# Kernel optimization log

Hardware: AMD Instinct MI355X
Metric: run time of the kernel (lower is better)

The kernel has to match this reference:

```python
import jax, jax.numpy as jnp
import numpy as np

D = 512
H = 8
HD = D // H
EPS = 1e-8


def setup_inputs() -> dict:
    key = jax.random.key(0)
    ks = jax.random.split(key, 16)
    B, S = 4, 2048
    s = lambda n: 1.0 / np.sqrt(n)
    inp = {
        "gene_emb": jax.random.normal(ks[0], (B, S, D), jnp.float32),
        "expr_emb": jax.random.normal(ks[1], (B, S, D), jnp.float32),
        "M": jax.random.uniform(ks[2], (B, S, S), jnp.float32),
        # weights stored (in, out) so y = x @ W + b
        "W_fused": jax.random.normal(ks[3], (2 * D, D), jnp.float32) * s(2 * D),
        "b_fused": jnp.zeros((D,), jnp.float32),
        "W_Q": jax.random.normal(ks[4], (D, D), jnp.float32) * s(D),
        "b_Q": jnp.zeros((D,), jnp.float32),
        "W_K": jax.random.normal(ks[5], (D, D), jnp.float32) * s(D),
        "b_K": jnp.zeros((D,), jnp.float32),
        "W_V": jax.random.normal(ks[6], (D, D), jnp.float32) * s(D),
        "b_V": jnp.zeros((D,), jnp.float32),
        "W_O": jax.random.normal(ks[7], (D, D), jnp.float32) * s(D),
        "b_O": jnp.zeros((D,), jnp.float32),
    }
    return inp


def reference(gene_emb, expr_emb, M, W_fused, b_fused, W_Q, b_Q, W_K, b_K, W_V, b_V, W_O, b_O):
    B, S, _ = gene_emb.shape
    scale = HD ** (-0.5)
    fused = jnp.concatenate([gene_emb, expr_emb], axis=-1) @ W_fused + b_fused
    # (B,S,D) -> (B,H,S,HD)
    split = lambda x: x.reshape(B, S, H, HD).transpose(0, 2, 1, 3)
    Q = split(fused @ W_Q + b_Q)
    K = split(fused @ W_K + b_K)
    V = split(expr_emb @ W_V + b_V)
    scores = jnp.einsum("bhqd,bhkd->bhqk", Q, K) * scale
    Mg = M[:, None, :, :]  # broadcast over heads
    scores = scores * Mg
    attn = jax.nn.softmax(scores, axis=-1)
    A_sparse = attn * Mg
    norm = jnp.sum(jnp.abs(A_sparse), axis=-1, keepdims=True) + EPS
    A_bar = A_sparse / norm
    out = jnp.einsum("bhqk,bhkd->bhqd", A_bar, V)
    out = out.transpose(0, 2, 1, 3).reshape(B, S, D)
    return out @ W_O + b_O
```

## Files before the change

kernel.cpp:

```cpp
#include <hip/hip_runtime.h>

typedef unsigned short u16;
typedef __attribute__((ext_vector_type(8))) short bf16x8_t;
typedef __attribute__((ext_vector_type(4))) float f32x4_t;

__device__ __forceinline__ u16 f2bf(float x){
  union { float f; unsigned u; } v; v.f = x;
  unsigned r = v.u + 0x7FFFu + ((v.u >> 16) & 1u);
  return (u16)(r >> 16);
}
__device__ __forceinline__ float bf2f(u16 h){
  union { unsigned u; float f; } v; v.u = ((unsigned)h) << 16;
  return v.f;
}
__device__ __forceinline__ unsigned pack_hi16(float a, float b){
  union { float f; unsigned u; } x, y; x.f = a; y.f = b;
  return (x.u >> 16) | (y.u & 0xFFFF0000u);
}

__device__ __forceinline__ void gl2lds16(const u16* g, u16* l){
  __builtin_amdgcn_global_load_lds((const __attribute__((address_space(1))) void*)g,
                                   (__attribute__((address_space(3))) void*)l, 16, 0, 0);
}

__global__ __launch_bounds__(256) void split_concat_kernel(
    const float* __restrict__ gene, const float* __restrict__ expr,
    u16* __restrict__ Xh, u16* __restrict__ Xl)
{
  size_t e = ((size_t)blockIdx.x * 256 + threadIdx.x) * 4;
  int row = (int)(e >> 10);
  int col = (int)(e & 1023);
  const float* src = (col < 512) ? (gene + (size_t)row * 512 + col)
                                 : (expr + (size_t)row * 512 + (col - 512));
  float4 v = *(const float4*)src;
  float a[4] = {v.x, v.y, v.z, v.w};
  u16 hs[4], ls[4];
#pragma unroll
  for (int i = 0; i < 4; i++){
    hs[i] = f2bf(a[i]);
    ls[i] = f2bf(a[i] - bf2f(hs[i]));
  }
  *(uint2*)(Xh + e) = make_uint2(hs[0] | ((unsigned)hs[1] << 16), hs[2] | ((unsigned)hs[3] << 16));
  *(uint2*)(Xl + e) = make_uint2(ls[0] | ((unsigned)ls[1] << 16), ls[2] | ((unsigned)ls[3] << 16));
}

__global__ __launch_bounds__(256) void transpose_all_kernel(
    const float* __restrict__ Wf, const float* __restrict__ Wq,
    const float* __restrict__ Wk, const float* __restrict__ Wv,
    const float* __restrict__ Wo,
    u16* __restrict__ Wfth, u16* __restrict__ Wftl,
    u16* __restrict__ Wqth, u16* __restrict__ Wkth,
    u16* __restrict__ Wvth, u16* __restrict__ Woth)
{
  __shared__ float t[64][65];
  int id = blockIdx.x;
  const float* W; u16* Th; u16* Tl; int K, kx, ny;
  if (id < 128){ W = Wf; Th = Wfth; Tl = Wftl; K = 1024; kx = id >> 3; ny = id & 7; }
  else {
    int tt = id - 128; int wi = tt >> 6; tt &= 63; kx = tt >> 3; ny = tt & 7; K = 512;
    W  = (wi == 0) ? Wq  : (wi == 1) ? Wk  : (wi == 2) ? Wv  : Wo;
    Th = (wi == 0) ? Wqth: (wi == 1) ? Wkth: (wi == 2) ? Wvth: Woth;
    Tl = nullptr;
  }
  int k0 = kx * 64, n0 = ny * 64;
  int tid = threadIdx.x;
  int r = tid >> 4;
  int c4 = (tid & 15) * 4;
#pragma unroll
  for (int p = 0; p < 4; p++){
    int k = p * 16 + r;
    float4 v = *(const float4*)(W + (size_t)(k0 + k) * 512 + n0 + c4);
    t[c4 + 0][k] = v.x; t[c4 + 1][k] = v.y; t[c4 + 2][k] = v.z; t[c4 + 3][k] = v.w;
  }
  __syncthreads();
#pragma unroll
  for (int p = 0; p < 4; p++){
    int n = p * 16 + r;
    u16 hs[4], ls[4];
#pragma unroll
    for (int i = 0; i < 4; i++){
      float x = t[n][c4 + i];
      hs[i] = f2bf(x);
      ls[i] = f2bf(x - bf2f(hs[i]));
    }
    size_t o = (size_t)(n0 + n) * K + k0 + c4;
    *(uint2*)(Th + o) = make_uint2(hs[0] | ((unsigned)hs[1] << 16), hs[2] | ((unsigned)hs[3] << 16));
    if (Tl)
      *(uint2*)(Tl + o) = make_uint2(ls[0] | ((unsigned)ls[1] << 16), ls[2] | ((unsigned)ls[3] << 16));
  }
}

template<int SPLITS, int MODE, int DUAL>
__global__ __launch_bounds__(256, 2) void gemm_kernel(
    const u16* __restrict__ Ah, const u16* __restrict__ Al, int lda,
    const u16* __restrict__ Bh0, const u16* __restrict__ Bl0,
    const u16* __restrict__ Bh1, int K,
    const float* __restrict__ bias0, const float* __restrict__ bias1,
    void* __restrict__ out0, void* __restrict__ out1, void* __restrict__ outsec,
    float sc0, float sc1)
{
  __shared__ __align__(16) u16 sAh[128 * 32];
  __shared__ __align__(16) u16 sAl[SPLITS >= 2 ? 128 * 32 : 8];
  __shared__ __align__(16) u16 sBh[64 * 32];
  __shared__ __align__(16) u16 sBl[SPLITS == 3 ? 64 * 32 : 8];
  int tid = threadIdx.x;
  int lane = tid & 63, w = tid >> 6, quad = lane >> 4, l15 = lane & 15;
  int wm = w & 1, wn = w >> 1;
  int m0 = blockIdx.x * 128;
  int side = DUAL ? (int)(blockIdx.y >> 3) : 0;
  int n0 = (DUAL ? (int)(blockIdx.y & 7) : (int)blockIdx.y) * 64;
  const u16* Bh = (DUAL && side) ? Bh1 : Bh0;
  const float* bias = (DUAL && side) ? bias1 : bias0;
  void* o0 = (DUAL && side) ? outsec : out0;
  float sc = (DUAL && side) ? sc1 : sc0;

  f32x4_t acc[4][2];
#pragma unroll
  for (int i = 0; i < 4; i++)
#pragma unroll
    for (int j = 0; j < 2; j++)
#pragma unroll
      for (int r = 0; r < 4; r++) acc[i][j][r] = 0.f;

  int lrow = lane >> 2;
  int swzS = ((lane >> 2) & 3) ^ ((lane >> 4) & 3);
  int gkq  = ((lane & 3) ^ swzS) * 8;
  const u16* pAh0 = Ah + (size_t)(m0 + w * 32 + lrow) * lda + gkq;
  const u16* pAh1 = Ah + (size_t)(m0 + w * 32 + 16 + lrow) * lda + gkq;
  const u16* pAl0 = (SPLITS >= 2) ? Al + (size_t)(m0 + w * 32 + lrow) * lda + gkq : nullptr;
  const u16* pAl1 = (SPLITS >= 2) ? Al + (size_t)(m0 + w * 32 + 16 + lrow) * lda + gkq : nullptr;
  const u16* pBh0 = Bh + (size_t)(n0 + w * 16 + lrow) * K + gkq;
  const u16* pBl0 = (SPLITS == 3) ? Bl0 + (size_t)(n0 + w * 16 + lrow) * K + gkq : nullptr;
  u16* dAh = sAh + w * 1024;
  u16* dAl = sAl + w * 1024;
  u16* dBh = sBh + w * 512;
  u16* dBl = sBl + w * 512;

  int pq = (quad ^ ((l15 & 3) ^ ((l15 >> 2) & 3))) * 8;

  for (int k0 = 0; k0 < K; k0 += 32){
    __syncthreads();
    gl2lds16(pAh0 + k0, dAh);
    gl2lds16(pAh1 + k0, dAh + 512);
    if constexpr (SPLITS >= 2){
      gl2lds16(pAl0 + k0, dAl);
      gl2lds16(pAl1 + k0, dAl + 512);
    }
    gl2lds16(pBh0 + k0, dBh);
    if constexpr (SPLITS == 3)
      gl2lds16(pBl0 + k0, dBl);
    __syncthreads();

    bf16x8_t aH[4], aL[4], bH[2], bL[2];
#pragma unroll
    for (int mi = 0; mi < 4; mi++){
      int ad = (wm * 64 + mi * 16 + l15) * 32 + pq;
      aH[mi] = *(const bf16x8_t*)&sAh[ad];
      if constexpr (SPLITS >= 2) aL[mi] = *(const bf16x8_t*)&sAl[ad];
    }
#pragma unroll
    for (int ni = 0; ni < 2; ni++){
      int bd = (wn * 32 + ni * 16 + l15) * 32 + pq;
      bH[ni] = *(const bf16x8_t*)&sBh[bd];
      if constexpr (SPLITS == 3) bL[ni] = *(const bf16x8_t*)&sBl[bd];
    }
#pragma unroll
    for (int mi = 0; mi < 4; mi++)
#pragma unroll
      for (int ni = 0; ni < 2; ni++){
        acc[mi][ni] = __builtin_amdgcn_mfma_f32_16x16x32_bf16(aH[mi], bH[ni], acc[mi][ni], 0, 0, 0);
        if constexpr (SPLITS == 3)
          acc[mi][ni] = __builtin_amdgcn_mfma_f32_16x16x32_bf16(aH[mi], bL[ni], acc[mi][ni], 0, 0, 0);
        if constexpr (SPLITS >= 2)
          acc[mi][ni] = __builtin_amdgcn_mfma_f32_16x16x32_bf16(aL[mi], bH[ni], acc[mi][ni], 0, 0, 0);
      }
  }

#pragma unroll
  for (int mi = 0; mi < 4; mi++)
#pragma unroll
    for (int ni = 0; ni < 2; ni++){
      int gn = n0 + wn * 32 + ni * 16 + l15;
      float bs = bias[gn];
      int gm0 = m0 + wm * 64 + mi * 16 + quad * 4;
#pragma unroll
      for (int r = 0; r < 4; r++){
        float v = acc[mi][ni][r] + bs;
        int gm = gm0 + r;
        if constexpr (MODE == 0){
          u16 hb = f2bf(v);
          ((u16*)o0)[(size_t)gm * 512 + gn] = hb;
          ((u16*)out1)[(size_t)gm * 512 + gn] = f2bf(v - bf2f(hb));
        } else if constexpr (MODE == 1){
          ((u16*)o0)[(size_t)gm * 512 + gn] = f2bf(v * sc);
        } else if constexpr (MODE == 2){
          int bb = gm >> 11, s = gm & 2047;
          int hh = gn >> 6, d = gn & 63;
          ((u16*)o0)[((size_t)((bb * 8 + hh) * 64 + d) << 11) + s] = f2bf(v);
        } else {
          ((float*)o0)[(size_t)gm * 512 + gn] = v;
        }
      }
    }
}

__global__ __launch_bounds__(256, 3) void flash_kernel(
    const u16* __restrict__ Qh, const u16* __restrict__ Kh,
    const u16* __restrict__ Vt, const float* __restrict__ Mm,
    u16* __restrict__ Oh)
{
  __shared__ __align__(16) u16 sKh[64 * 64], sVt[64 * 64];
  int tid = threadIdx.x, lane = tid & 63, w = tid >> 6, quad = lane >> 4, l15 = lane & 15;
  int bh = blockIdx.y, b = bh >> 3, h = bh & 7;
  int q0 = blockIdx.x * 64;
  int q = q0 + w * 16 + l15;

  const u16* qp = Qh + ((size_t)(b * 2048 + q)) * 512 + h * 64 + quad * 8;
  bf16x8_t qH[2];
  qH[0] = *(const bf16x8_t*)qp;
  qH[1] = *(const bf16x8_t*)(qp + 32);

  int srow = lane >> 3;
  int gc = ((lane & 7) ^ (srow & 7)) * 8;
  const u16* gKh0 = Kh + ((size_t)(b * 2048 + w * 16 + srow)) * 512 + h * 64 + gc;
  const u16* gVt0 = Vt + ((size_t)(bh * 64 + w * 16 + srow)) * 2048 + gc;
  u16* dKh = sKh + w * 1024;
  u16* dVt = sVt + w * 1024;

  const float* mp = Mm + (size_t)b * (2048 * 2048) + (size_t)q * 2048 + quad * 8;

  float lp = 0.f;
  f32x4_t Oacc[4];
#pragma unroll
  for (int dn = 0; dn < 4; dn++)
#pragma unroll
    for (int r = 0; r < 4; r++) Oacc[dn][r] = 0.f;

  float Mc[2][8];
#pragma unroll
  for (int pt = 0; pt < 2; pt++){
    *(f32x4_t*)&Mc[pt][0] = *(const f32x4_t*)(mp + pt * 32);
    *(f32x4_t*)&Mc[pt][4] = *(const f32x4_t*)(mp + pt * 32 + 4);
  }

  int khi = l15 >> 2;
  int klo2 = (l15 & 3) * 2;
  int vlo = l15 & 7;
  int vhi = l15 >> 3;

  for (int k0 = 0; k0 < 2048; k0 += 64){
    __syncthreads();
    gl2lds16(gKh0 + (size_t)k0 * 512,       dKh);
    gl2lds16(gKh0 + (size_t)(k0 + 8) * 512, dKh + 512);
    gl2lds16(gVt0 + k0,                     dVt);
    gl2lds16(gVt0 + 8 * 2048 + k0,          dVt + 512);
    __syncthreads();

    float Mn[2][8];
    bool hasNext = (k0 + 64) < 2048;
    if (hasNext){
#pragma unroll
      for (int pt = 0; pt < 2; pt++){
        *(f32x4_t*)&Mn[pt][0] = *(const f32x4_t*)(mp + (k0 + 64) + pt * 32);
        *(f32x4_t*)&Mn[pt][4] = *(const f32x4_t*)(mp + (k0 + 64) + pt * 32 + 4);
      }
    }

    f32x4_t S[2][2];
#pragma unroll
    for (int pt = 0; pt < 2; pt++)
#pragma unroll
      for (int t = 0; t < 2; t++){
        int sr = klo2 + t;
        int base = (pt * 4 + khi) * 512 + sr * 64;
        f32x4_t s;
#pragma unroll
        for (int r = 0; r < 4; r++) s[r] = 0.f;
#pragma unroll
        for (int ds = 0; ds < 2; ds++){
          bf16x8_t kf = *(const bf16x8_t*)&sKh[base + (((ds * 4 + quad) ^ sr)) * 8];
          s = __builtin_amdgcn_mfma_f32_16x16x32_bf16(kf, qH[ds], s, 0, 0, 0);
        }
        S[pt][t] = s;
      }

#pragma unroll
    for (int pt = 0; pt < 2; pt++){
      float p[2][4];
#pragma unroll
      for (int t = 0; t < 2; t++)
#pragma unroll
        for (int r = 0; r < 4; r++){
          float m = Mc[pt][2 * r + t];
          float v = m * __builtin_amdgcn_exp2f(S[pt][t][r] * m);
          lp += v;
          p[t][r] = v;
        }
      union { unsigned u[4]; bf16x8_t v8; } pb;
#pragma unroll
      for (int r = 0; r < 4; r++)
        pb.u[r] = pack_hi16(p[0][r], p[1][r]);
#pragma unroll
      for (int dn = 0; dn < 4; dn++){
        bf16x8_t vf = *(const bf16x8_t*)&sVt[(dn * 2 + vhi) * 512 + vlo * 64 + (((pt * 4 + quad) ^ vlo)) * 8];
        Oacc[dn] = __builtin_amdgcn_mfma_f32_16x16x32_bf16(vf, pb.v8, Oacc[dn], 0, 0, 0);
      }
    }

    if (hasNext){
#pragma unroll
      for (int pt = 0; pt < 2; pt++)
#pragma unroll
        for (int j = 0; j < 8; j++) Mc[pt][j] = Mn[pt][j];
    }
  }

  lp += __shfl_xor(lp, 16);
  lp += __shfl_xor(lp, 32);
  float inv = 1.0f / lp;

  size_t ob = ((size_t)(b * 2048 + q)) * 512 + h * 64 + quad * 4;
#pragma unroll
  for (int dn = 0; dn < 4; dn++){
    unsigned w0 = (unsigned)f2bf(Oacc[dn][0] * inv) | ((unsigned)f2bf(Oacc[dn][1] * inv) << 16);
    unsigned w1 = (unsigned)f2bf(Oacc[dn][2] * inv) | ((unsigned)f2bf(Oacc[dn][3] * inv) << 16);
    *(uint2*)(Oh + ob + dn * 16) = make_uint2(w0, w1);
  }
}

extern "C" void kernel_launch(void* const* d_in, const int* in_sizes, int n_in,
                              void* d_out, int out_size, void* d_ws, size_t ws_size,
                              hipStream_t stream)
{
  const float* gene = (const float*)d_in[0];
  const float* expr = (const float*)d_in[1];
  const float* Mm   = (const float*)d_in[2];
  const float* Wf   = (const float*)d_in[3];
  const float* bfv  = (const float*)d_in[4];
  const float* Wq   = (const float*)d_in[5];
  const float* bq   = (const float*)d_in[6];
  const float* Wk   = (const float*)d_in[7];
  const float* bk   = (const float*)d_in[8];
  const float* Wv   = (const float*)d_in[9];
  const float* bv   = (const float*)d_in[10];
  const float* Wo   = (const float*)d_in[11];
  const float* bo   = (const float*)d_in[12];
  float* out = (float*)d_out;

  char* ws = (char*)d_ws;
  size_t off = 0;
  auto alloc = [&](size_t bytes) -> void* {
    void* p = (void*)(ws + off);
    off += (bytes + 255) & ~(size_t)255;
    return p;
  };
  u16* Xh   = (u16*)alloc(8192ull * 1024 * 2);
  u16* Xl   = (u16*)alloc(8192ull * 1024 * 2);
  u16* Wfth = (u16*)alloc(512ull * 1024 * 2);
  u16* Wftl = (u16*)alloc(512ull * 1024 * 2);
  u16* Wqth = (u16*)alloc(512ull * 512 * 2);
  u16* Wkth = (u16*)alloc(512ull * 512 * 2);
  u16* Wvth = (u16*)alloc(512ull * 512 * 2);
  u16* Woth = (u16*)alloc(512ull * 512 * 2);
  u16* Fh   = (u16*)alloc(8192ull * 512 * 2);
  u16* Fl   = (u16*)alloc(8192ull * 512 * 2);
  u16* Qh   = (u16*)alloc(8192ull * 512 * 2);
  u16* Kh   = (u16*)alloc(8192ull * 512 * 2);
  u16* Vt   = (u16*)alloc(8192ull * 512 * 2);
  u16* Oh = Xh;

  const float QSC = 0.1803368801f;

  split_concat_kernel<<<8192, 256, 0, stream>>>(gene, expr, Xh, Xl);
  transpose_all_kernel<<<384, 256, 0, stream>>>(Wf, Wq, Wk, Wv, Wo,
                                                Wfth, Wftl, Wqth, Wkth, Wvth, Woth);

  gemm_kernel<3, 0, 0><<<dim3(64, 8), 256, 0, stream>>>(
      Xh, Xl, 1024, Wfth, Wftl, nullptr, 1024, bfv, nullptr, Fh, Fl, nullptr, 1.f, 1.f);
  gemm_kernel<2, 1, 1><<<dim3(64, 16), 256, 0, stream>>>(
      Fh, Fl, 512, Wqth, nullptr, Wkth, 512, bq, bk, Qh, nullptr, Kh, QSC, 1.f);
  gemm_kernel<2, 2, 0><<<dim3(64, 8), 256, 0, stream>>>(
      Xh + 512, Xl + 512, 1024, Wvth, nullptr, nullptr, 512, bv, nullptr, Vt, nullptr, nullptr, 1.f, 1.f);
  flash_kernel<<<dim3(32, 32), 256, 0, stream>>>(Qh, Kh, Vt, Mm, Oh);
  gemm_kernel<1, 3, 0><<<dim3(64, 8), 256, 0, stream>>>(
      Oh, nullptr, 512, Woth, nullptr, nullptr, 512, bo, nullptr, out, nullptr, nullptr, 1.f, 1.f);

  (void)in_sizes; (void)n_in; (void)out_size; (void)ws_size;
}
```

Baseline: 317.4 us.

## Process two heads per flash block and double-buffer K/V tiles in LDS

Each flash-attention block now handles two heads for the same query tile. The mask M is shared across heads, so each mask load serves both heads, which halves mask traffic (the mask is the largest input). K/V staging becomes double-buffered: the next tile's global-to-LDS copy is issued before computing the current one, leaving one barrier per step. The costs are a larger LDS footprint (64KB), more registers, a launch bound reduced to 2 blocks per CU, and half as many blocks in the grid.

```diff
diff --git a/kernel.cpp b/kernel.cpp
--- a/kernel.cpp
+++ b/kernel.cpp
@@ -204,127 +204,165 @@
     }
 }
 
-__global__ __launch_bounds__(256, 3) void flash_kernel(
+__global__ __launch_bounds__(256, 2) void flash_kernel(
     const u16* __restrict__ Qh, const u16* __restrict__ Kh,
     const u16* __restrict__ Vt, const float* __restrict__ Mm,
     u16* __restrict__ Oh)
 {
-  __shared__ __align__(16) u16 sKh[64 * 64], sVt[64 * 64];
+  __shared__ __align__(16) u16 sK[2][8192];
+  __shared__ __align__(16) u16 sV[2][8192];
   int tid = threadIdx.x, lane = tid & 63, w = tid >> 6, quad = lane >> 4, l15 = lane & 15;
-  int bh = blockIdx.y, b = bh >> 3, h = bh & 7;
+  int by = blockIdx.y, b = by >> 2, j = by & 3;
+  int h0 = 2 * j;
   int q0 = blockIdx.x * 64;
   int q = q0 + w * 16 + l15;
 
-  const u16* qp = Qh + ((size_t)(b * 2048 + q)) * 512 + h * 64 + quad * 8;
-  bf16x8_t qH[2];
-  qH[0] = *(const bf16x8_t*)qp;
-  qH[1] = *(const bf16x8_t*)(qp + 32);
-
-  int srow = lane >> 3;
-  int gc = ((lane & 7) ^ (srow & 7)) * 8;
-  const u16* gKh0 = Kh + ((size_t)(b * 2048 + w * 16 + srow)) * 512 + h * 64 + gc;
-  const u16* gVt0 = Vt + ((size_t)(bh * 64 + w * 16 + srow)) * 2048 + gc;
-  u16* dKh = sKh + w * 1024;
-  u16* dVt = sVt + w * 1024;
+  const u16* qp = Qh + ((size_t)(b * 2048 + q)) * 512 + h0 * 64 + quad * 8;
+  bf16x8_t qH[2][2];
+#pragma unroll
+  for (int hh = 0; hh < 2; hh++){
+    qH[hh][0] = *(const bf16x8_t*)(qp + hh * 64);
+    qH[hh][1] = *(const bf16x8_t*)(qp + hh * 64 + 32);
+  }
+
+  int srow = lane >> 3, c8 = lane & 7;
+  const u16* gKa0 = Kh + ((size_t)(b * 2048 + w * 16 + srow)) * 512 + h0 * 64
+                       + ((c8 ^ srow ^ ((w * 2) & 3)) << 3);
+  const u16* gKa1 = Kh + ((size_t)(b * 2048 + w * 16 + 8 + srow)) * 512 + h0 * 64
+                       + ((c8 ^ srow ^ ((w * 2 + 1) & 3)) << 3);
+  const u16* gVa0 = Vt + ((size_t)((b * 8 + h0) * 64 + w * 16 + srow)) * 2048
+                       + ((c8 ^ srow) << 3);
+  u16* dK = &sK[0][0] + w * 1024;
+  u16* dV = &sV[0][0] + w * 1024;
+  const int BUFSTRIDE = 8192;
 
   const float* mp = Mm + (size_t)b * (2048 * 2048) + (size_t)q * 2048 + quad * 8;
 
-  float lp = 0.f;
-  f32x4_t Oacc[4];
-#pragma unroll
-  for (int dn = 0; dn < 4; dn++)
-#pragma unroll
-    for (int r = 0; r < 4; r++) Oacc[dn][r] = 0.f;
-
-  float Mc[2][8];
-#pragma unroll
-  for (int pt = 0; pt < 2; pt++){
-    *(f32x4_t*)&Mc[pt][0] = *(const f32x4_t*)(mp + pt * 32);
-    *(f32x4_t*)&Mc[pt][4] = *(const f32x4_t*)(mp + pt * 32 + 4);
-  }
+  float lp[2] = {0.f, 0.f};
+  f32x4_t Oacc[2][4];
+#pragma unroll
+  for (int hh = 0; hh < 2; hh++)
+#pragma unroll
+    for (int dn = 0; dn < 4; dn++)
+#pragma unroll
+      for (int r = 0; r < 4; r++) Oacc[hh][dn][r] = 0.f;
 
   int khi = l15 >> 2;
   int klo2 = (l15 & 3) * 2;
   int vlo = l15 & 7;
   int vhi = l15 >> 3;
 
-  for (int k0 = 0; k0 < 2048; k0 += 64){
-    __syncthreads();
-    gl2lds16(gKh0 + (size_t)k0 * 512,       dKh);
-    gl2lds16(gKh0 + (size_t)(k0 + 8) * 512, dKh + 512);
-    gl2lds16(gVt0 + k0,                     dVt);
-    gl2lds16(gVt0 + 8 * 2048 + k0,          dVt + 512);
-    __syncthreads();
-
-    float Mn[2][8];
-    bool hasNext = (k0 + 64) < 2048;
-    if (hasNext){
-#pragma unroll
-      for (int pt = 0; pt < 2; pt++){
-        *(f32x4_t*)&Mn[pt][0] = *(const f32x4_t*)(mp + (k0 + 64) + pt * 32);
-        *(f32x4_t*)&Mn[pt][4] = *(const f32x4_t*)(mp + (k0 + 64) + pt * 32 + 4);
+#define STAGE_KV(B, K0) do {                                                    \
+    int kk = (K0);                                                              \
+    gl2lds16(gKa0 + (size_t)kk * 512,            dK + (B) * BUFSTRIDE);         \
+    gl2lds16(gKa1 + (size_t)kk * 512,            dK + (B) * BUFSTRIDE + 512);   \
+    gl2lds16(gKa0 + 64 + (size_t)kk * 512,       dK + (B) * BUFSTRIDE + 4096);  \
+    gl2lds16(gKa1 + 64 + (size_t)kk * 512,       dK + (B) * BUFSTRIDE + 4608);  \
+    gl2lds16(gVa0 + kk,                          dV + (B) * BUFSTRIDE);         \
+    gl2lds16(gVa0 + 8 * 2048 + kk,               dV + (B) * BUFSTRIDE + 512);   \
+    gl2lds16(gVa0 + 64 * 2048 + kk,              dV + (B) * BUFSTRIDE + 4096);  \
+    gl2lds16(gVa0 + 64 * 2048 + 8 * 2048 + kk,   dV + (B) * BUFSTRIDE + 4608);  \
+  } while (0)
+
+  STAGE_KV(0, 0);
+  float Mc[2][8];
+#pragma unroll
+  for (int pt = 0; pt < 2; pt++){
+    *(f32x4_t*)&Mc[pt][0] = *(const f32x4_t*)(mp + pt * 32);
+    *(f32x4_t*)&Mc[pt][4] = *(const f32x4_t*)(mp + pt * 32 + 4);
+  }
+  __syncthreads();
+
+  for (int tt = 0; tt < 16; ++tt){
+#pragma unroll
+    for (int ph = 0; ph < 2; ++ph){
+      int t = tt * 2 + ph;
+      bool hasNext = t < 31;
+      if (hasNext) STAGE_KV(ph ^ 1, (t + 1) * 64);
+
+      float Mn[2][8];
+      if (hasNext){
+        int kn = (t + 1) * 64;
+#pragma unroll
+        for (int pt = 0; pt < 2; pt++){
+          *(f32x4_t*)&Mn[pt][0] = *(const f32x4_t*)(mp + kn + pt * 32);
+          *(f32x4_t*)&Mn[pt][4] = *(const f32x4_t*)(mp + kn + pt * 32 + 4);
+        }
       }
-    }
-
-    f32x4_t S[2][2];
-#pragma unroll
-    for (int pt = 0; pt < 2; pt++)
-#pragma unroll
-      for (int t = 0; t < 2; t++){
-        int sr = klo2 + t;
-        int base = (pt * 4 + khi) * 512 + sr * 64;
-        f32x4_t s;
-#pragma unroll
-        for (int r = 0; r < 4; r++) s[r] = 0.f;
-#pragma unroll
-        for (int ds = 0; ds < 2; ds++){
-          bf16x8_t kf = *(const bf16x8_t*)&sKh[base + (((ds * 4 + quad) ^ sr)) * 8];
-          s = __builtin_amdgcn_mfma_f32_16x16x32_bf16(kf, qH[ds], s, 0, 0, 0);
+
+#pragma unroll
+      for (int hh = 0; hh < 2; ++hh){
+        const u16* kb = &sK[ph][hh * 4096];
+        const u16* vb = &sV[ph][hh * 4096];
+
+        f32x4_t S[2][2];
+#pragma unroll
+        for (int pt = 0; pt < 2; pt++)
+#pragma unroll
+          for (int t2 = 0; t2 < 2; t2++){
+            int sr = klo2 + t2;
+            int rb = (pt * 4 + khi) * 512 + sr * 64;
+            f32x4_t s;
+#pragma unroll
+            for (int r = 0; r < 4; r++) s[r] = 0.f;
+#pragma unroll
+            for (int ds = 0; ds < 2; ds++){
+              bf16x8_t kf = *(const bf16x8_t*)&kb[rb + (((ds * 4 + quad) ^ sr ^ khi)) * 8];
+              s = __builtin_amdgcn_mfma_f32_16x16x32_bf16(kf, qH[hh][ds], s, 0, 0, 0);
+            }
+            S[pt][t2] = s;
+          }
+
+#pragma unroll
+        for (int pt = 0; pt < 2; pt++){
+          float p[2][4];
+#pragma unroll
+          for (int t2 = 0; t2 < 2; t2++)
+#pragma unroll
+            for (int r = 0; r < 4; r++){
+              float m = Mc[pt][2 * r + t2];
+              float v = m * __builtin_amdgcn_exp2f(S[pt][t2][r] * m);
+              lp[hh] += v;
+              p[t2][r] = v;
+            }
+          union { unsigned u[4]; bf16x8_t v8; } pb;
+#pragma unroll
+          for (int r = 0; r < 4; r++)
+            pb.u[r] = pack_hi16(p[0][r], p[1][r]);
+#pragma unroll
+          for (int dn = 0; dn < 4; dn++){
+            bf16x8_t vf = *(const bf16x8_t*)&vb[(dn * 2 + vhi) * 512 + vlo * 64
+                                               + (((pt * 4 + quad) ^ vlo)) * 8];
+            Oacc[hh][dn] = __builtin_amdgcn_mfma_f32_16x16x32_bf16(vf, pb.v8, Oacc[hh][dn], 0, 0, 0);
+          }
         }
-        S[pt][t] = s;
       }
 
-#pragma unroll
-    for (int pt = 0; pt < 2; pt++){
-      float p[2][4];
-#pragma unroll
-      for (int t = 0; t < 2; t++)
-#pragma unroll
-        for (int r = 0; r < 4; r++){
-          float m = Mc[pt][2 * r + t];
-          float v = m * __builtin_amdgcn_exp2f(S[pt][t][r] * m);
-          lp += v;
-          p[t][r] = v;
-        }
-      union { unsigned u[4]; bf16x8_t v8; } pb;
-#pragma unroll
-      for (int r = 0; r < 4; r++)
-        pb.u[r] = pack_hi16(p[0][r], p[1][r]);
-#pragma unroll
-      for (int dn = 0; dn < 4; dn++){
-        bf16x8_t vf = *(const bf16x8_t*)&sVt[(dn * 2 + vhi) * 512 + vlo * 64 + (((pt * 4 + quad) ^ vlo)) * 8];
-        Oacc[dn] = __builtin_amdgcn_mfma_f32_16x16x32_bf16(vf, pb.v8, Oacc[dn], 0, 0, 0);
+      __syncthreads();
+
+      if (hasNext){
+#pragma unroll
+        for (int pt = 0; pt < 2; pt++)
+#pragma unroll
+          for (int e = 0; e < 8; e++) Mc[pt][e] = Mn[pt][e];
       }
     }
-
-    if (hasNext){
-#pragma unroll
-      for (int pt = 0; pt < 2; pt++)
-#pragma unroll
-        for (int j = 0; j < 8; j++) Mc[pt][j] = Mn[pt][j];
-    }
-  }
-
-  lp += __shfl_xor(lp, 16);
-  lp += __shfl_xor(lp, 32);
-  float inv = 1.0f / lp;
-
-  size_t ob = ((size_t)(b * 2048 + q)) * 512 + h * 64 + quad * 4;
-#pragma unroll
-  for (int dn = 0; dn < 4; dn++){
-    unsigned w0 = (unsigned)f2bf(Oacc[dn][0] * inv) | ((unsigned)f2bf(Oacc[dn][1] * inv) << 16);
-    unsigned w1 = (unsigned)f2bf(Oacc[dn][2] * inv) | ((unsigned)f2bf(Oacc[dn][3] * inv) << 16);
-    *(uint2*)(Oh + ob + dn * 16) = make_uint2(w0, w1);
+  }
+#undef STAGE_KV
+
+#pragma unroll
+  for (int hh = 0; hh < 2; ++hh){
+    float l = lp[hh];
+    l += __shfl_xor(l, 16);
+    l += __shfl_xor(l, 32);
+    float inv = 1.0f / l;
+    size_t ob = ((size_t)(b * 2048 + q)) * 512 + (h0 + hh) * 64 + quad * 4;
+#pragma unroll
+    for (int dn = 0; dn < 4; dn++){
+      unsigned w0 = (unsigned)f2bf(Oacc[hh][dn][0] * inv) | ((unsigned)f2bf(Oacc[hh][dn][1] * inv) << 16);
+      unsigned w1 = (unsigned)f2bf(Oacc[hh][dn][2] * inv) | ((unsigned)f2bf(Oacc[hh][dn][3] * inv) << 16);
+      *(uint2*)(Oh + ob + dn * 16) = make_uint2(w0, w1);
+    }
   }
 }
 
@@ -381,7 +419,7 @@
       Fh, Fl, 512, Wqth, nullptr, Wkth, 512, bq, bk, Qh, nullptr, Kh, QSC, 1.f);
   gemm_kernel<2, 2, 0><<<dim3(64, 8), 256, 0, stream>>>(
       Xh + 512, Xl + 512, 1024, Wvth, nullptr, nullptr, 512, bv, nullptr, Vt, nullptr, nullptr, 1.f, 1.f);
-  flash_kernel<<<dim3(32, 32), 256, 0, stream>>>(Qh, Kh, Vt, Mm, Oh);
+  flash_kernel<<<dim3(32, 16), 256, 0, stream>>>(Qh, Kh, Vt, Mm, Oh);
   gemm_kernel<1, 3, 0><<<dim3(64, 8), 256, 0, stream>>>(
       Oh, nullptr, 512, Woth, nullptr, nullptr, 512, bo, nullptr, out, nullptr, nullptr, 1.f, 1.f);
 
```

After: 308.2 us. -2.9%, faster.
